# Kernel optimization log

Measured on AMD Instinct MI355X. Metric: run time of the kernel, lower is better.

## Reference

```python
import jax, jax.numpy as jnp
import numpy as np

V = 30000      # vocab_size
D = 300        # t_embed
H = 4          # GATv2 heads
C = 300        # per-head out channels (hidden_dim = t_embed)
HID = 768      # hidden_size
B = 2
T = 800
NEG = 0.2      # GATv2 negative_slope default


def gatv2_layer(x, src, dst, Wl, bl, Wr, br, att, bias):
    """PyG GATv2Conv, eval mode, add_self_loops=True, concat=True.
    x: [N, Fin]; src/dst: [E] (src->dst message flow).
    Wl/Wr: [Fin, H*C]; bl/br: [H*C]; att: [H, C]; bias: [H*C].
    """
    N = x.shape[0]
    xl = (x @ Wl + bl).reshape(N, H, C)   # source transform
    xr = (x @ Wr + br).reshape(N, H, C)   # target transform
    loops = jnp.arange(N)
    s = jnp.concatenate([src, loops])
    d = jnp.concatenate([dst, loops])
    e = jax.nn.leaky_relu(xl[s] + xr[d], NEG)          # [E', H, C]
    logits = jnp.einsum('ehc,hc->eh', e, att)           # [E', H]
    # scatter-softmax over incoming edges per target node
    mx = jax.ops.segment_max(logits, d, num_segments=N)  # [N, H]
    ex = jnp.exp(logits - mx[d])
    den = jax.ops.segment_sum(ex, d, num_segments=N)
    alpha = ex / den[d]                                   # [E', H]
    out = jax.ops.segment_sum(alpha[:, :, None] * xl[s], d, num_segments=N)
    return out.reshape(N, H * C) + bias


def setup_inputs() -> dict:
    key = jax.random.key(0)
    ks = jax.random.split(key, 20)
    sc = 0.05
    inp = {
        'kg_enc_input': jax.random.randint(ks[0], (B, T, 3), 0, V),
        'embeddings': jax.random.normal(ks[1], (V, D), jnp.float32),
        # conv1: GATv2Conv(D, C, heads=H)
        'Wl1': jax.random.normal(ks[2], (D, H * C), jnp.float32) * sc,
        'bl1': jnp.zeros((H * C,), jnp.float32),
        'Wr1': jax.random.normal(ks[3], (D, H * C), jnp.float32) * sc,
        'br1': jnp.zeros((H * C,), jnp.float32),
        'att1': jax.random.normal(ks[4], (H, C), jnp.float32) * sc,
        'bias1': jnp.zeros((H * C,), jnp.float32),
        # conv2: GATv2Conv(4*C, C, heads=H)
        'Wl2': jax.random.normal(ks[5], (H * C, H * C), jnp.float32) * sc,
        'bl2': jnp.zeros((H * C,), jnp.float32),
        'Wr2': jax.random.normal(ks[6], (H * C, H * C), jnp.float32) * sc,
        'br2': jnp.zeros((H * C,), jnp.float32),
        'att2': jax.random.normal(ks[7], (H, C), jnp.float32) * sc,
        'bias2': jnp.zeros((H * C,), jnp.float32),
        # post_mp: Linear(4*C, C) -> Dropout -> Linear(C, D)
        'Wp1': jax.random.normal(ks[8], (H * C, C), jnp.float32) * sc,
        'bp1': jnp.zeros((C,), jnp.float32),
        'Wp2': jax.random.normal(ks[9], (C, D), jnp.float32) * sc,
        'bp2': jnp.zeros((D,), jnp.float32),
        # lii: Linear(3*D, HID, bias=False)
        'Wlii': jax.random.normal(ks[10], (3 * D, HID), jnp.float32) * sc,
    }
    return inp


def reference(kg_enc_input, embeddings, Wl1, bl1, Wr1, br1, att1, bias1,
              Wl2, bl2, Wr2, br2, att2, bias2, Wp1, bp1, Wp2, bp2, Wlii):
    # original GAT.forward detaches x -> no grad to embedding table
    x0 = jax.lax.stop_gradient(embeddings)

    def per_sample(kg):  # kg: [T, 3]
        head, rel, tail = kg[:, 0], kg[:, 1], kg[:, 2]
        # edge_list = cat([[head;rel], [rel;tail]], dim=1)
        src = jnp.concatenate([head, rel])
        dst = jnp.concatenate([rel, tail])
        h = gatv2_layer(x0, src, dst, Wl1, bl1, Wr1, br1, att1, bias1)
        h = jax.nn.relu(h)                 # dropout: eval mode, identity
        h = gatv2_layer(h, src, dst, Wl2, bl2, Wr2, br2, att2, bias2)
        h = jax.nn.relu(h)
        w = (h @ Wp1 + bp1) @ Wp2 + bp2    # post_mp, [V, D]
        # per-triple gather + concat of (h, r, t) node embeddings
        return jnp.concatenate([w[head], w[rel], w[tail]], axis=-1)  # [T, 3D]

    final = jax.vmap(per_sample)(kg_enc_input)   # [B, T, 3D]
    return final @ Wlii                           # [B, T, HID]
```

## Files before the change

kernel.cpp:

```cpp
#include <hip/hip_runtime.h>
#include <hip/hip_bf16.h>

#define V 30000
#define D 300
#define H 4
#define C 300
#define HC 1200
#define B 2
#define T 800
#define E 1600
#define MAXM 2400
#define NEG 0.2f
#define SCAN_CH ((MAXM + 255) / 256)

#define MR 2432
#define KD 320
#define KHC 1216
#define NLR 2432
#define WB_LD 320
#define KF2 960
#define FRW 896

typedef __attribute__((ext_vector_type(8))) unsigned short u16x8;
typedef __attribute__((ext_vector_type(8))) short s16x8;
typedef __attribute__((ext_vector_type(4))) float f32x4;

__device__ inline unsigned short f2b(float v) {
    unsigned u = __float_as_uint(v);
    unsigned r = (u + 0x7FFFu + ((u >> 16) & 1u)) >> 16;
    return (unsigned short)r;
}
__device__ inline float b2f(unsigned short u) {
    return __uint_as_float(((unsigned)u) << 16);
}

#define GLOAD_LDS16(g, l) __builtin_amdgcn_global_load_lds( \
    (const __attribute__((address_space(1))) void*)(g), \
    (__attribute__((address_space(3))) void*)(l), 16, 0, 0)


__global__ void k_init(int* map, int* list, int* deg, int* fill, int* mcnt) {
    int i = blockIdx.x * blockDim.x + threadIdx.x;
    if (i < B * V) map[i] = -1;
    if (i < B * MAXM) { list[i] = 0; deg[i] = 0; fill[i] = 0; }
    if (i < B) mcnt[i] = 0;
}

__global__ void k_mark(const int* __restrict__ kg, int* map) {
    int i = blockIdx.x * blockDim.x + threadIdx.x;
    if (i >= B * T * 3) return;
    int b = i / (T * 3);
    map[b * V + kg[i]] = 1;
}

__global__ void k_compact(int* map, int* list, int* mcnt) {
    int b = blockIdx.y;
    int i = blockIdx.x * 256 + threadIdx.x;
    bool pred = (i < V) && (map[b * V + i] == 1);
    unsigned long long m = __ballot(pred);
    int lane = threadIdx.x & 63;
    int wid = threadIdx.x >> 6;
    __shared__ int wcnt[4];
    __shared__ int base;
    if (lane == 0) wcnt[wid] = __popcll(m);
    __syncthreads();
    if (threadIdx.x == 0) {
        int t = 0;
#pragma unroll
        for (int w2 = 0; w2 < 4; ++w2) { int c = wcnt[w2]; wcnt[w2] = t; t += c; }
        base = t ? atomicAdd(&mcnt[b], t) : 0;
    }
    __syncthreads();
    if (pred) {
        int idx = base + wcnt[wid] + __popcll(m & ((1ull << lane) - 1ull));
        map[b * V + i] = idx;
        list[b * MAXM + idx] = i;
    }
}

__global__ void k_edges(const int* __restrict__ kg, const int* __restrict__ map,
                        int* esrc, int* edst, int* deg, int* tric) {
    int i = blockIdx.x * blockDim.x + threadIdx.x;
    if (i >= B * T) return;
    int b = i / T, t = i % T;
    const int* kk = kg + ((long)b * T + t) * 3;
    int hc = map[b * V + kk[0]];
    int rc = map[b * V + kk[1]];
    int tc = map[b * V + kk[2]];
    int eb = b * E;
    esrc[eb + t]     = hc;  edst[eb + t]     = rc;
    esrc[eb + T + t] = rc;  edst[eb + T + t] = tc;
    atomicAdd(&deg[b * MAXM + rc], 1);
    atomicAdd(&deg[b * MAXM + tc], 1);
    int* tr = tric + ((long)b * T + t) * 3;
    tr[0] = hc; tr[1] = rc; tr[2] = tc;
}

__global__ void k_scan(const int* __restrict__ deg, int* __restrict__ off) {
    int b = blockIdx.x;
    deg += b * MAXM; off += b * (MAXM + 1);
    __shared__ int ts[256];
    int t = threadIdx.x;
    int base = t * SCAN_CH;
    int loc[SCAN_CH];
    int sum = 0;
#pragma unroll
    for (int j = 0; j < SCAN_CH; ++j) {
        int v = (base + j < MAXM) ? deg[base + j] : 0;
        sum += v; loc[j] = sum;
    }
    ts[t] = sum; __syncthreads();
    for (int s = 1; s < 256; s <<= 1) {
        int v = (t >= s) ? ts[t - s] : 0;
        __syncthreads();
        ts[t] += v;
        __syncthreads();
    }
    int excl = (t > 0) ? ts[t - 1] : 0;
#pragma unroll
    for (int j = 0; j < SCAN_CH; ++j)
        if (base + j < MAXM) off[base + j + 1] = excl + loc[j];
    if (t == 0) off[0] = 0;
}

__global__ void k_scatter(const int* __restrict__ esrc, const int* __restrict__ edst,
                          const int* __restrict__ off, int* fill, int* csr) {
    int i = blockIdx.x * blockDim.x + threadIdx.x;
    if (i >= B * E) return;
    int b = i / E;
    int d = edst[i];
    int pos = off[b * (MAXM + 1) + d] + atomicAdd(&fill[b * MAXM + d], 1);
    csr[b * E + pos] = esrc[i];
}

__global__ void k_wt_all(const float* __restrict__ Wl1, const float* __restrict__ Wr1,
                         const float* __restrict__ Wl2, const float* __restrict__ Wr2,
                         const float* __restrict__ Wp1, const float* __restrict__ Wp2,
                         const float* __restrict__ Wlii,
                         const float* __restrict__ bl1, const float* __restrict__ br1,
                         const float* __restrict__ bl2, const float* __restrict__ br2,
                         const float* __restrict__ bp1, const float* __restrict__ bp2,
                         unsigned short* Wlr1t, unsigned short* Wlr2t,
                         unsigned short* Wp2t, unsigned short* Wp1b,
                         unsigned short* Wft2,
                         float* blr1, float* blr2, float* bp12) {
    const int KT[6]  = {10, 10, 38, 38, 10, 30};
    const int CUM[10] = {0, 380, 760, 2204, 3648, 3748, 4468, 4508, 4518, 4520};
    int bid = blockIdx.x;
    int task = 0;
    while (bid >= CUM[task + 1]) ++task;
    int local = bid - CUM[task];
    int tx = threadIdx.x, ty = threadIdx.y;
    int tid = ty * 32 + tx;

    if (task == 6) {
        int r0 = local * 32;
#pragma unroll
        for (int p = 0; p < 4; ++p) {
            int row = r0 + ty + p * 8;
#pragma unroll
            for (int j = 0; j < 10; ++j) {
                int c = tx + j * 32;
                unsigned short v = 0;
                if (row < 1200 && c < 300) v = f2b(Wp1[(long)row * 300 + c]);
                Wp1b[(long)row * 320 + c] = v;
            }
        }
        return;
    }
    if (task == 7) {
        int c = local * 256 + tid;
        if (c < NLR) {
            float v1 = 0.f, v2 = 0.f;
            if (c < 1200) { v1 = bl1[c]; v2 = bl2[c]; }
            else if (c >= 1216 && c < 2416) { v1 = br1[c - 1216]; v2 = br2[c - 1216]; }
            blr1[c] = v1; blr2[c] = v2;
        }
        return;
    }
    if (task == 8) {
        int n = local * 256 + tid;
        if (n < 300) {
            float s = bp2[n];
            for (int m = 0; m < 300; ++m) s += bp1[m] * Wp2[(long)m * 300 + n];
            bp12[n] = s;
        }
        return;
    }

    __shared__ float t[32][33];
    if (task == 5) {
        int kt = local % 30, nt = local / 30;
        int k0 = kt * 32, n0 = nt * 32;
#pragma unroll
        for (int p = 0; p < 4; ++p) {
            int gk = k0 + ty + p * 8, n = n0 + tx;
            int pp = (gk >= 640) ? 2 : (gk >= 320 ? 1 : 0);
            int kc = gk - pp * 320;
            t[ty + p * 8][tx] = (kc < 300) ? Wlii[(long)(300 * pp + kc) * 768 + n] : 0.f;
        }
        __syncthreads();
#pragma unroll
        for (int p = 0; p < 4; ++p) {
            int n = n0 + ty + p * 8, gk = k0 + tx;
            Wft2[(long)n * 960 + gk] = f2b(t[tx][ty + p * 8]);
        }
        return;
    }

    int kt = local % KT[task], nt = local / KT[task];
    const float* W; unsigned short* Wt; int K, N, Kp;
    switch (task) {
        case 0: W = Wl1;  Wt = Wlr1t;                     K = 300;  N = 1200; Kp = KD;  break;
        case 1: W = Wr1;  Wt = Wlr1t + (long)1216 * KD;   K = 300;  N = 1200; Kp = KD;  break;
        case 2: W = Wl2;  Wt = Wlr2t;                     K = 1200; N = 1200; Kp = KHC; break;
        case 3: W = Wr2;  Wt = Wlr2t + (long)1216 * KHC;  K = 1200; N = 1200; Kp = KHC; break;
        default: W = Wp2; Wt = Wp2t;                      K = 300;  N = 300;  Kp = KD;  break;
    }
    int k0 = kt * 32, n0 = nt * 32;
#pragma unroll
    for (int p = 0; p < 4; ++p) {
        int k = k0 + ty + p * 8, n = n0 + tx;
        t[ty + p * 8][tx] = (k < K && n < N) ? W[(long)k * N + n] : 0.f;
    }
    __syncthreads();
#pragma unroll
    for (int p = 0; p < 4; ++p) {
        int n = n0 + ty + p * 8, k = k0 + tx;
        Wt[(long)n * Kp + k] = f2b(t[tx][ty + p * 8]);
    }
}

__global__ void k_embgather(const float* __restrict__ emb, const int* __restrict__ list,
                            unsigned short* __restrict__ Eb) {
    int b = blockIdx.y, i = blockIdx.x;
    int src = list[b * MAXM + i];
    const float* e = emb + (long)src * D;
    unsigned short* o = Eb + ((long)b * MR + i) * KD;
    int c = threadIdx.x;
    if (c < 75) {
        float4 v = *(const float4*)(e + c * 4);
        ushort4 u;
        u.x = f2b(v.x); u.y = f2b(v.y); u.z = f2b(v.z); u.w = f2b(v.w);
        *(ushort4*)(o + c * 4) = u;
    } else if (c < 80) {
        *(ushort4*)(o + c * 4) = make_ushort4(0, 0, 0, 0);
    }
}

__device__ inline void tile_decode(int& m0, int& n0) {
    int nbx = gridDim.x, nby = gridDim.y;
    int nwg = nbx * nby;
    int wg = blockIdx.y * nbx + blockIdx.x;
    int q = nwg >> 3, r8 = nwg & 7;
    int xcd = wg & 7, idx = wg >> 3;
    int L = (xcd < r8 ? xcd * (q + 1) : r8 * (q + 1) + (xcd - r8) * q) + idx;
    const int G = 4;
    int band = L / (G * nbx);
    int first = band * G;
    int sz = min(G, nby - first);
    int rem = L - band * G * nbx;
    int by = first + rem % sz;
    int bx = rem / sz;
    m0 = by * 128; n0 = bx * 128;
}

__global__ __launch_bounds__(256) void k_mgemm(
    const unsigned short* __restrict__ A, long sA, int lda,
    const unsigned short* __restrict__ Wt, int ldw,
    const float* __restrict__ bias,
    int M, int N, int K,
    float* __restrict__ outF, long sF, int ldf,
    unsigned short* __restrict__ outB, long sB, int ldb_) {
    int b = blockIdx.z;
    A += (long)b * sA;
    __shared__ unsigned short As[128][32];
    __shared__ unsigned short Bs[128][32];
    int tid = threadIdx.x;
    int m0, n0; tile_decode(m0, n0);

    int w = tid >> 6, lane = tid & 63;
    int wr = (w >> 1) * 64, wc = (w & 1) * 64;
    int fr = lane & 15, fq = lane >> 4;
    int r0 = tid >> 2, sg = tid & 3;
    int swz = (sg ^ ((r0 >> 1) & 3)) * 8;
    const unsigned short* Ap  = A  + (long)(m0 + r0) * lda + swz;
    const unsigned short* Ap2 = A  + (long)(m0 + r0 + 64) * lda + swz;
    const unsigned short* Bp  = Wt + (long)(n0 + r0) * ldw + swz;
    const unsigned short* Bp2 = Wt + (long)(n0 + r0 + 64) * ldw + swz;
    unsigned short* lA  = &As[r0][sg * 8];
    unsigned short* lA2 = &As[r0 + 64][sg * 8];
    unsigned short* lB  = &Bs[r0][sg * 8];
    unsigned short* lB2 = &Bs[r0 + 64][sg * 8];

    f32x4 acc[4][4] = {};
    for (int k0 = 0; k0 < K; k0 += 32) {
        GLOAD_LDS16(Ap + k0, lA);
        GLOAD_LDS16(Ap2 + k0, lA2);
        GLOAD_LDS16(Bp + k0, lB);
        GLOAD_LDS16(Bp2 + k0, lB2);
        __syncthreads();
        s16x8 af[4], bfr[4];
#pragma unroll
        for (int m = 0; m < 4; ++m) {
            int rr = wr + m * 16 + fr;
            af[m] = *(const s16x8*)&As[rr][(fq ^ ((rr >> 1) & 3)) * 8];
        }
#pragma unroll
        for (int n = 0; n < 4; ++n) {
            int rr = wc + n * 16 + fr;
            bfr[n] = *(const s16x8*)&Bs[rr][(fq ^ ((rr >> 1) & 3)) * 8];
        }
#pragma unroll
        for (int m = 0; m < 4; ++m)
#pragma unroll
            for (int n = 0; n < 4; ++n)
                acc[m][n] = __builtin_amdgcn_mfma_f32_16x16x32_bf16(af[m], bfr[n], acc[m][n], 0, 0, 0);
        __syncthreads();
    }
    float* oF = outF ? outF + (long)b * sF : nullptr;
    unsigned short* oB = outB ? outB + (long)b * sB : nullptr;
#pragma unroll
    for (int m = 0; m < 4; ++m) {
        int rb = m0 + wr + m * 16 + fq * 4;
#pragma unroll
        for (int n = 0; n < 4; ++n) {
            int col = n0 + wc + n * 16 + fr;
#pragma unroll
            for (int j = 0; j < 4; ++j) {
                int row = rb + j;
                if (row >= M) continue;
                if (col < N) {
                    float v = acc[m][n][j] + (bias ? bias[col] : 0.f);
                    if (oF) oF[(long)row * ldf + col] = v;
                    if (oB) oB[(long)row * ldb_ + col] = f2b(v);
                } else if (oB && col < ldb_) {
                    oB[(long)row * ldb_ + col] = 0;
                }
            }
        }
    }
}

__global__ __launch_bounds__(256) void k_fgemm(
    const unsigned short* __restrict__ wb, long sW,
    const int* __restrict__ tric,
    const unsigned short* __restrict__ Wft2,
    float* __restrict__ out) {
    int b = blockIdx.z;
    const unsigned short* wB = wb + (long)b * sW;
    const int* tr = tric + (long)b * T * 3;
    float* oF = out + (long)b * T * 768;
    __shared__ unsigned short As[128][32];
    __shared__ unsigned short Bs[128][32];
    int tid = threadIdx.x;
    int m0, n0; tile_decode(m0, n0);

    int w = tid >> 6, lane = tid & 63;
    int wr = (w >> 1) * 64, wc = (w & 1) * 64;
    int fr = lane & 15, fq = lane >> 4;
    int r0 = tid >> 2, sg = tid & 3;
    int swz = (sg ^ ((r0 >> 1) & 3)) * 8;

    int gm  = m0 + r0;
    int gm2 = gm + 64;
    int t1 = min(gm, T - 1) * 3, t2 = min(gm2, T - 1) * 3;
    int tr0a = tr[t1], tr1a = tr[t1 + 1], tr2a = tr[t1 + 2];
    int tr0b = tr[t2], tr1b = tr[t2 + 1], tr2b = tr[t2 + 2];

    const unsigned short* Bp  = Wft2 + (long)(n0 + r0) * KF2 + swz;
    const unsigned short* Bp2 = Wft2 + (long)(n0 + r0 + 64) * KF2 + swz;
    unsigned short* lA  = &As[r0][sg * 8];
    unsigned short* lA2 = &As[r0 + 64][sg * 8];
    unsigned short* lB  = &Bs[r0][sg * 8];
    unsigned short* lB2 = &Bs[r0 + 64][sg * 8];

    f32x4 acc[4][4] = {};
    for (int k0 = 0; k0 < KF2; k0 += 32) {
        int kk = k0 + swz;
        int p_ = (kk >= 640) ? 2 : (kk >= 320 ? 1 : 0);
        int kc = kk - p_ * 320;
        int tA  = (p_ == 0) ? tr0a : (p_ == 1 ? tr1a : tr2a);
        int tA2 = (p_ == 0) ? tr0b : (p_ == 1 ? tr1b : tr2b);
        GLOAD_LDS16(wB + (long)tA * WB_LD + kc, lA);
        GLOAD_LDS16(wB + (long)tA2 * WB_LD + kc, lA2);
        GLOAD_LDS16(Bp + k0, lB);
        GLOAD_LDS16(Bp2 + k0, lB2);
        __syncthreads();
        s16x8 af[4], bfr[4];
#pragma unroll
        for (int m = 0; m < 4; ++m) {
            int rr = wr + m * 16 + fr;
            af[m] = *(const s16x8*)&As[rr][(fq ^ ((rr >> 1) & 3)) * 8];
        }
#pragma unroll
        for (int n = 0; n < 4; ++n) {
            int rr = wc + n * 16 + fr;
            bfr[n] = *(const s16x8*)&Bs[rr][(fq ^ ((rr >> 1) & 3)) * 8];
        }
#pragma unroll
        for (int m = 0; m < 4; ++m)
#pragma unroll
            for (int n = 0; n < 4; ++n)
                acc[m][n] = __builtin_amdgcn_mfma_f32_16x16x32_bf16(af[m], bfr[n], acc[m][n], 0, 0, 0);
        __syncthreads();
    }
#pragma unroll
    for (int m = 0; m < 4; ++m) {
        int rb = m0 + wr + m * 16 + fq * 4;
#pragma unroll
        for (int n = 0; n < 4; ++n) {
            int col = n0 + wc + n * 16 + fr;
#pragma unroll
            for (int j = 0; j < 4; ++j) {
                int row = rb + j;
                if (row < T) oF[(long)row * 768 + col] = acc[m][n][j];
            }
        }
    }
}

__global__ __launch_bounds__(256) void k_att(
    const unsigned short* __restrict__ XLR,
    const int* __restrict__ deg, const int* __restrict__ off, const int* __restrict__ csr,
    const float* __restrict__ att, const float* __restrict__ bias,
    unsigned short* __restrict__ OUT) {
    const long sX = (long)MR * NLR;
    const long sO = (long)MR * KHC;
    int b = blockIdx.y;
    int i = blockIdx.x;
    const unsigned short* xl = XLR + (long)b * sX;
    const unsigned short* xr = xl + 1216;
    unsigned short* out = OUT + (long)b * sO;
    int lane = threadIdx.x & 63;
    int h = threadIdx.x >> 6;
    int c0 = lane * 4;
    int c1 = 256 + c0;
    bool tail = lane < 11;

    float xrf[8], attf[8];
    {
        const unsigned short* xp = xr + (long)i * NLR + h * C;
        ushort4 u0 = *(const ushort4*)(xp + c0);
        ushort4 u1 = tail ? *(const ushort4*)(xp + c1) : make_ushort4(0, 0, 0, 0);
        xrf[0] = b2f(u0.x); xrf[1] = b2f(u0.y); xrf[2] = b2f(u0.z); xrf[3] = b2f(u0.w);
        xrf[4] = b2f(u1.x); xrf[5] = b2f(u1.y); xrf[6] = b2f(u1.z); xrf[7] = b2f(u1.w);
        float4 a0 = *(const float4*)(att + h * C + c0);
        attf[0] = a0.x; attf[1] = a0.y; attf[2] = a0.z; attf[3] = a0.w;
        if (tail) {
            float4 a1 = *(const float4*)(att + h * C + c1);
            attf[4] = a1.x; attf[5] = a1.y; attf[6] = a1.z; attf[7] = a1.w;
        } else { attf[4] = attf[5] = attf[6] = attf[7] = 0.f; }
    }
    int dg = deg[b * MAXM + i];
    int o0 = off[b * (MAXM + 1) + i];
    const int* cs = csr + b * E;

    float mx = -3e38f, den = 0.f;
    float acc[8] = {0.f, 0.f, 0.f, 0.f, 0.f, 0.f, 0.f, 0.f};
    auto step = [&](int s) {
        const unsigned short* xp = xl + (long)s * NLR + h * C;
        ushort4 v0 = *(const ushort4*)(xp + c0);
        ushort4 v1 = tail ? *(const ushort4*)(xp + c1) : make_ushort4(0, 0, 0, 0);
        float xv[8];
        xv[0] = b2f(v0.x); xv[1] = b2f(v0.y); xv[2] = b2f(v0.z); xv[3] = b2f(v0.w);
        xv[4] = b2f(v1.x); xv[5] = b2f(v1.y); xv[6] = b2f(v1.z); xv[7] = b2f(v1.w);
        float part = 0.f;
#pragma unroll
        for (int j = 0; j < 8; ++j) {
            float v = xv[j] + xrf[j];
            v = v > 0.f ? v : NEG * v;
            part += attf[j] * v;
        }
#pragma unroll
        for (int m = 1; m < 64; m <<= 1) part += __shfl_xor(part, m);
        float mn = fmaxf(mx, part);
        float sc = __expf(mx - mn);
        float p = __expf(part - mn);
        den = den * sc + p;
#pragma unroll
        for (int j = 0; j < 8; ++j) acc[j] = acc[j] * sc + p * xv[j];
        mx = mn;
    };
    step(i);
    for (int e = 0; e < dg; ++e) step(cs[o0 + e]);

    float inv = 1.f / den;
    unsigned short* op = out + (long)i * KHC + h * C;
    {
        float4 b0 = *(const float4*)(bias + h * C + c0);
        ushort4 s0;
        float v;
        v = acc[0] * inv + b0.x; s0.x = f2b(v > 0.f ? v : 0.f);
        v = acc[1] * inv + b0.y; s0.y = f2b(v > 0.f ? v : 0.f);
        v = acc[2] * inv + b0.z; s0.z = f2b(v > 0.f ? v : 0.f);
        v = acc[3] * inv + b0.w; s0.w = f2b(v > 0.f ? v : 0.f);
        *(ushort4*)(op + c0) = s0;
        if (tail) {
            float4 b1 = *(const float4*)(bias + h * C + c1);
            ushort4 s1;
            v = acc[4] * inv + b1.x; s1.x = f2b(v > 0.f ? v : 0.f);
            v = acc[5] * inv + b1.y; s1.y = f2b(v > 0.f ? v : 0.f);
            v = acc[6] * inv + b1.z; s1.z = f2b(v > 0.f ? v : 0.f);
            v = acc[7] * inv + b1.w; s1.w = f2b(v > 0.f ? v : 0.f);
            *(ushort4*)(op + c1) = s1;
        }
    }
    if (h == 0 && lane < KHC - HC)
        out[(long)i * KHC + HC + lane] = 0;
}

extern "C" void kernel_launch(void* const* d_in, const int* in_sizes, int n_in,
                              void* d_out, int out_size, void* d_ws, size_t ws_size,
                              hipStream_t stream) {
    const int*   kg    = (const int*)d_in[0];
    const float* emb   = (const float*)d_in[1];
    const float* Wl1   = (const float*)d_in[2];
    const float* bl1   = (const float*)d_in[3];
    const float* Wr1   = (const float*)d_in[4];
    const float* br1   = (const float*)d_in[5];
    const float* att1  = (const float*)d_in[6];
    const float* bias1 = (const float*)d_in[7];
    const float* Wl2   = (const float*)d_in[8];
    const float* bl2   = (const float*)d_in[9];
    const float* Wr2   = (const float*)d_in[10];
    const float* br2   = (const float*)d_in[11];
    const float* att2  = (const float*)d_in[12];
    const float* bias2 = (const float*)d_in[13];
    const float* Wp1   = (const float*)d_in[14];
    const float* bp1   = (const float*)d_in[15];
    const float* Wp2   = (const float*)d_in[16];
    const float* bp2   = (const float*)d_in[17];
    const float* Wlii  = (const float*)d_in[18];
    float* out = (float*)d_out;

    char* ws = (char*)d_ws;
    size_t o = 0;
    auto alloc = [&](size_t bytes) -> void* {
        void* p = ws + o;
        o = (o + bytes + 255) & ~(size_t)255;
        return p;
    };
    int* map  = (int*)alloc(sizeof(int) * B * V);
    int* list = (int*)alloc(sizeof(int) * B * MAXM);
    int* mcnt = (int*)alloc(sizeof(int) * B);
    int* deg  = (int*)alloc(sizeof(int) * B * MAXM);
    int* off  = (int*)alloc(sizeof(int) * B * (MAXM + 1));
    int* fill = (int*)alloc(sizeof(int) * B * MAXM);
    int* esrc = (int*)alloc(sizeof(int) * B * E);
    int* edst = (int*)alloc(sizeof(int) * B * E);
    int* csr  = (int*)alloc(sizeof(int) * B * E);
    int* tric = (int*)alloc(sizeof(int) * B * T * 3);

    long sXlr = (long)MR * NLR;
    long sHb  = (long)MR * KHC;
    long sEb  = (long)MR * KD;
    unsigned short* Xlr = (unsigned short*)alloc(2LL * B * sXlr);
    unsigned short* Hb  = (unsigned short*)alloc(2LL * B * sHb);
    unsigned short* Eb  = (unsigned short*)alloc(2LL * B * sEb);

    unsigned short* Wlr1t = (unsigned short*)alloc(2LL * 2432 * KD);
    unsigned short* Wlr2t = (unsigned short*)alloc(2LL * 2432 * KHC);
    unsigned short* Wp2t  = (unsigned short*)alloc(2LL * 384 * KD);
    unsigned short* Wp1b  = (unsigned short*)alloc(2LL * 1280 * 320);
    unsigned short* Wp12t = (unsigned short*)alloc(2LL * 384 * KHC);
    unsigned short* Wft2  = (unsigned short*)alloc(2LL * 768 * KF2);
    float* blr1 = (float*)alloc(sizeof(float) * NLR);
    float* blr2 = (float*)alloc(sizeof(float) * NLR);
    float* bp12 = (float*)alloc(sizeof(float) * 384);
    (void)ws_size; (void)in_sizes; (void)n_in; (void)out_size;

    unsigned short* wb = Eb;

    k_init<<<(B * V + 255) / 256, 256, 0, stream>>>(map, list, deg, fill, mcnt);
    k_mark<<<(B * T * 3 + 255) / 256, 256, 0, stream>>>(kg, map);
    k_compact<<<dim3((V + 255) / 256, B), 256, 0, stream>>>(map, list, mcnt);
    k_edges<<<(B * T + 255) / 256, 256, 0, stream>>>(kg, map, esrc, edst, deg, tric);
    k_scan<<<B, 256, 0, stream>>>(deg, off);
    k_scatter<<<(B * E + 255) / 256, 256, 0, stream>>>(esrc, edst, off, fill, csr);

    k_wt_all<<<4520, dim3(32, 8), 0, stream>>>(Wl1, Wr1, Wl2, Wr2, Wp1, Wp2, Wlii,
                                               bl1, br1, bl2, br2, bp1, bp2,
                                               Wlr1t, Wlr2t, Wp2t, Wp1b, Wft2,
                                               blr1, blr2, bp12);

    k_embgather<<<dim3(MAXM, B), 128, 0, stream>>>(emb, list, Eb);

    k_mgemm<<<dim3(10, 3, 1), 256, 0, stream>>>(Wp2t, 0, KD, Wp1b, 320, nullptr,
                                                300, 1216, KD,
                                                nullptr, 0, 0, Wp12t, 0, KHC);

    long sWb = (long)MR * WB_LD;

    dim3 gL(19, 19, B);
    k_mgemm<<<gL, 256, 0, stream>>>(Eb, sEb, KD, Wlr1t, KD, blr1, MAXM, NLR, KD,
                                    nullptr, 0, 0, Xlr, sXlr, NLR);
    k_att<<<dim3(MAXM, B), 256, 0, stream>>>(Xlr, deg, off, csr, att1, bias1, Hb);
    k_mgemm<<<gL, 256, 0, stream>>>(Hb, sHb, KHC, Wlr2t, KHC, blr2, MAXM, NLR, KHC,
                                    nullptr, 0, 0, Xlr, sXlr, NLR);
    k_att<<<dim3(MAXM, B), 256, 0, stream>>>(Xlr, deg, off, csr, att2, bias2, Hb);
    k_mgemm<<<dim3(3, 19, B), 256, 0, stream>>>(Hb, sHb, KHC, Wp12t, KHC, bp12,
                                                MAXM, 300, KHC,
                                                nullptr, 0, 0, wb, sWb, WB_LD);
    k_fgemm<<<dim3(6, 7, B), 256, 0, stream>>>(wb, sWb, tric, Wft2, out);
}
```

Baseline: 346.4 us.

## Fuse graph CSR build into one kernel and double-buffer GEMM LDS tiles

Replaces the separate edge, scan and scatter kernels with one per-batch kernel that builds degrees, offsets and the CSR in shared memory, which drops two launches and the global atomics and buffers. The attention kernel now derives degree from consecutive offsets. Both GEMM kernels switch to double-buffered LDS so the next K-slice's global-to-LDS loads are issued before computing on the current one, aiming to overlap memory latency with MFMA work. This doubles LDS use per block, which may lower occupancy, and the fused graph kernel runs on only B blocks.

```diff
diff --git a/kernel.cpp b/kernel.cpp
--- a/kernel.cpp
+++ b/kernel.cpp
@@ -19,7 +19,6 @@
 #define NLR 2432
 #define WB_LD 320
 #define KF2 960
-#define FRW 896
 
 typedef __attribute__((ext_vector_type(8))) unsigned short u16x8;
 typedef __attribute__((ext_vector_type(8))) short s16x8;
@@ -39,10 +38,10 @@
     (__attribute__((address_space(3))) void*)(l), 16, 0, 0)
 
 
-__global__ void k_init(int* map, int* list, int* deg, int* fill, int* mcnt) {
+__global__ void k_init(int* map, int* list, int* mcnt) {
     int i = blockIdx.x * blockDim.x + threadIdx.x;
     if (i < B * V) map[i] = -1;
-    if (i < B * MAXM) { list[i] = 0; deg[i] = 0; fill[i] = 0; }
+    if (i < B * MAXM) list[i] = 0;
     if (i < B) mcnt[i] = 0;
 }
 
@@ -78,59 +77,62 @@
     }
 }
 
-__global__ void k_edges(const int* __restrict__ kg, const int* __restrict__ map,
-                        int* esrc, int* edst, int* deg, int* tric) {
-    int i = blockIdx.x * blockDim.x + threadIdx.x;
-    if (i >= B * T) return;
-    int b = i / T, t = i % T;
-    const int* kk = kg + ((long)b * T + t) * 3;
-    int hc = map[b * V + kk[0]];
-    int rc = map[b * V + kk[1]];
-    int tc = map[b * V + kk[2]];
-    int eb = b * E;
-    esrc[eb + t]     = hc;  edst[eb + t]     = rc;
-    esrc[eb + T + t] = rc;  edst[eb + T + t] = tc;
-    atomicAdd(&deg[b * MAXM + rc], 1);
-    atomicAdd(&deg[b * MAXM + tc], 1);
-    int* tr = tric + ((long)b * T + t) * 3;
-    tr[0] = hc; tr[1] = rc; tr[2] = tc;
-}
-
-__global__ void k_scan(const int* __restrict__ deg, int* __restrict__ off) {
+__global__ __launch_bounds__(256) void k_graph(const int* __restrict__ kg,
+                                               const int* __restrict__ map,
+                                               int* __restrict__ off_g,
+                                               int* __restrict__ csr,
+                                               int* __restrict__ tric) {
     int b = blockIdx.x;
-    deg += b * MAXM; off += b * (MAXM + 1);
+    int tid = threadIdx.x;
+    __shared__ int sdeg[MAXM];
+    __shared__ int soff[MAXM + 1];
+    __shared__ int ses[E];
+    __shared__ int sed[E];
     __shared__ int ts[256];
-    int t = threadIdx.x;
-    int base = t * SCAN_CH;
+    for (int j = tid; j < MAXM; j += 256) sdeg[j] = 0;
+    __syncthreads();
+    for (int t = tid; t < T; t += 256) {
+        const int* kk = kg + ((long)b * T + t) * 3;
+        int hc = map[b * V + kk[0]];
+        int rc = map[b * V + kk[1]];
+        int tc = map[b * V + kk[2]];
+        ses[t] = hc;     sed[t] = rc;
+        ses[T + t] = rc; sed[T + t] = tc;
+        atomicAdd(&sdeg[rc], 1);
+        atomicAdd(&sdeg[tc], 1);
+        int* tr = tric + ((long)b * T + t) * 3;
+        tr[0] = hc; tr[1] = rc; tr[2] = tc;
+    }
+    __syncthreads();
+    int base = tid * SCAN_CH;
     int loc[SCAN_CH];
     int sum = 0;
 #pragma unroll
     for (int j = 0; j < SCAN_CH; ++j) {
-        int v = (base + j < MAXM) ? deg[base + j] : 0;
+        int v = (base + j < MAXM) ? sdeg[base + j] : 0;
         sum += v; loc[j] = sum;
     }
-    ts[t] = sum; __syncthreads();
+    ts[tid] = sum; __syncthreads();
     for (int s = 1; s < 256; s <<= 1) {
-        int v = (t >= s) ? ts[t - s] : 0;
+        int v = (tid >= s) ? ts[tid - s] : 0;
         __syncthreads();
-        ts[t] += v;
+        ts[tid] += v;
         __syncthreads();
     }
-    int excl = (t > 0) ? ts[t - 1] : 0;
+    int excl = (tid > 0) ? ts[tid - 1] : 0;
 #pragma unroll
     for (int j = 0; j < SCAN_CH; ++j)
-        if (base + j < MAXM) off[base + j + 1] = excl + loc[j];
-    if (t == 0) off[0] = 0;
-}
-
-__global__ void k_scatter(const int* __restrict__ esrc, const int* __restrict__ edst,
-                          const int* __restrict__ off, int* fill, int* csr) {
-    int i = blockIdx.x * blockDim.x + threadIdx.x;
-    if (i >= B * E) return;
-    int b = i / E;
-    int d = edst[i];
-    int pos = off[b * (MAXM + 1) + d] + atomicAdd(&fill[b * MAXM + d], 1);
-    csr[b * E + pos] = esrc[i];
+        if (base + j < MAXM) soff[base + j + 1] = excl + loc[j];
+    if (tid == 0) soff[0] = 0;
+    __syncthreads();
+    for (int j = tid; j < MAXM; j += 256) sdeg[j] = 0;
+    __syncthreads();
+    for (int e = tid; e < E; e += 256) {
+        int d = sed[e];
+        int pos = soff[d] + atomicAdd(&sdeg[d], 1);
+        csr[b * E + pos] = ses[e];
+    }
+    for (int j = tid; j <= MAXM; j += 256) off_g[b * (MAXM + 1) + j] = soff[j];
 }
 
 __global__ void k_wt_all(const float* __restrict__ Wl1, const float* __restrict__ Wr1,
@@ -274,8 +276,8 @@
     unsigned short* __restrict__ outB, long sB, int ldb_) {
     int b = blockIdx.z;
     A += (long)b * sA;
-    __shared__ unsigned short As[128][32];
-    __shared__ unsigned short Bs[128][32];
+    __shared__ unsigned short As[2][128][32];
+    __shared__ unsigned short Bs[2][128][32];
     int tid = threadIdx.x;
     int m0, n0; tile_decode(m0, n0);
 
@@ -288,28 +290,32 @@
     const unsigned short* Ap2 = A  + (long)(m0 + r0 + 64) * lda + swz;
     const unsigned short* Bp  = Wt + (long)(n0 + r0) * ldw + swz;
     const unsigned short* Bp2 = Wt + (long)(n0 + r0 + 64) * ldw + swz;
-    unsigned short* lA  = &As[r0][sg * 8];
-    unsigned short* lA2 = &As[r0 + 64][sg * 8];
-    unsigned short* lB  = &Bs[r0][sg * 8];
-    unsigned short* lB2 = &Bs[r0 + 64][sg * 8];
 
     f32x4 acc[4][4] = {};
+    GLOAD_LDS16(Ap,  &As[0][r0][sg * 8]);
+    GLOAD_LDS16(Ap2, &As[0][r0 + 64][sg * 8]);
+    GLOAD_LDS16(Bp,  &Bs[0][r0][sg * 8]);
+    GLOAD_LDS16(Bp2, &Bs[0][r0 + 64][sg * 8]);
+    __syncthreads();
+    int cur = 0;
     for (int k0 = 0; k0 < K; k0 += 32) {
-        GLOAD_LDS16(Ap + k0, lA);
-        GLOAD_LDS16(Ap2 + k0, lA2);
-        GLOAD_LDS16(Bp + k0, lB);
-        GLOAD_LDS16(Bp2 + k0, lB2);
-        __syncthreads();
+        int nxt = cur ^ 1;
+        if (k0 + 32 < K) {
+            GLOAD_LDS16(Ap + k0 + 32,  &As[nxt][r0][sg * 8]);
+            GLOAD_LDS16(Ap2 + k0 + 32, &As[nxt][r0 + 64][sg * 8]);
+            GLOAD_LDS16(Bp + k0 + 32,  &Bs[nxt][r0][sg * 8]);
+            GLOAD_LDS16(Bp2 + k0 + 32, &Bs[nxt][r0 + 64][sg * 8]);
+        }
         s16x8 af[4], bfr[4];
 #pragma unroll
         for (int m = 0; m < 4; ++m) {
             int rr = wr + m * 16 + fr;
-            af[m] = *(const s16x8*)&As[rr][(fq ^ ((rr >> 1) & 3)) * 8];
+            af[m] = *(const s16x8*)&As[cur][rr][(fq ^ ((rr >> 1) & 3)) * 8];
         }
 #pragma unroll
         for (int n = 0; n < 4; ++n) {
             int rr = wc + n * 16 + fr;
-            bfr[n] = *(const s16x8*)&Bs[rr][(fq ^ ((rr >> 1) & 3)) * 8];
+            bfr[n] = *(const s16x8*)&Bs[cur][rr][(fq ^ ((rr >> 1) & 3)) * 8];
         }
 #pragma unroll
         for (int m = 0; m < 4; ++m)
@@ -317,6 +323,7 @@
             for (int n = 0; n < 4; ++n)
                 acc[m][n] = __builtin_amdgcn_mfma_f32_16x16x32_bf16(af[m], bfr[n], acc[m][n], 0, 0, 0);
         __syncthreads();
+        cur = nxt;
     }
     float* oF = outF ? outF + (long)b * sF : nullptr;
     unsigned short* oB = outB ? outB + (long)b * sB : nullptr;
@@ -351,8 +358,8 @@
     const unsigned short* wB = wb + (long)b * sW;
     const int* tr = tric + (long)b * T * 3;
     float* oF = out + (long)b * T * 768;
-    __shared__ unsigned short As[128][32];
-    __shared__ unsigned short Bs[128][32];
+    __shared__ unsigned short As[2][128][32];
+    __shared__ unsigned short Bs[2][128][32];
     int tid = threadIdx.x;
     int m0, n0; tile_decode(m0, n0);
 
@@ -365,38 +372,39 @@
     int gm  = m0 + r0;
     int gm2 = gm + 64;
     int t1 = min(gm, T - 1) * 3, t2 = min(gm2, T - 1) * 3;
-    int tr0a = tr[t1], tr1a = tr[t1 + 1], tr2a = tr[t1 + 2];
-    int tr0b = tr[t2], tr1b = tr[t2 + 1], tr2b = tr[t2 + 2];
+    int tr_a[3] = {tr[t1], tr[t1 + 1], tr[t1 + 2]};
+    int tr_b[3] = {tr[t2], tr[t2 + 1], tr[t2 + 2]};
 
     const unsigned short* Bp  = Wft2 + (long)(n0 + r0) * KF2 + swz;
     const unsigned short* Bp2 = Wft2 + (long)(n0 + r0 + 64) * KF2 + swz;
-    unsigned short* lA  = &As[r0][sg * 8];
-    unsigned short* lA2 = &As[r0 + 64][sg * 8];
-    unsigned short* lB  = &Bs[r0][sg * 8];
-    unsigned short* lB2 = &Bs[r0 + 64][sg * 8];
-
-    f32x4 acc[4][4] = {};
-    for (int k0 = 0; k0 < KF2; k0 += 32) {
+
+    auto stage = [&](int buf, int k0) {
         int kk = k0 + swz;
         int p_ = (kk >= 640) ? 2 : (kk >= 320 ? 1 : 0);
         int kc = kk - p_ * 320;
-        int tA  = (p_ == 0) ? tr0a : (p_ == 1 ? tr1a : tr2a);
-        int tA2 = (p_ == 0) ? tr0b : (p_ == 1 ? tr1b : tr2b);
-        GLOAD_LDS16(wB + (long)tA * WB_LD + kc, lA);
-        GLOAD_LDS16(wB + (long)tA2 * WB_LD + kc, lA2);
-        GLOAD_LDS16(Bp + k0, lB);
-        GLOAD_LDS16(Bp2 + k0, lB2);
-        __syncthreads();
+        GLOAD_LDS16(wB + (long)tr_a[p_] * WB_LD + kc, &As[buf][r0][sg * 8]);
+        GLOAD_LDS16(wB + (long)tr_b[p_] * WB_LD + kc, &As[buf][r0 + 64][sg * 8]);
+        GLOAD_LDS16(Bp + k0,  &Bs[buf][r0][sg * 8]);
+        GLOAD_LDS16(Bp2 + k0, &Bs[buf][r0 + 64][sg * 8]);
+    };
+
+    f32x4 acc[4][4] = {};
+    stage(0, 0);
+    __syncthreads();
+    int cur = 0;
+    for (int k0 = 0; k0 < KF2; k0 += 32) {
+        int nxt = cur ^ 1;
+        if (k0 + 32 < KF2) stage(nxt, k0 + 32);
         s16x8 af[4], bfr[4];
 #pragma unroll
         for (int m = 0; m < 4; ++m) {
             int rr = wr + m * 16 + fr;
-            af[m] = *(const s16x8*)&As[rr][(fq ^ ((rr >> 1) & 3)) * 8];
+            af[m] = *(const s16x8*)&As[cur][rr][(fq ^ ((rr >> 1) & 3)) * 8];
         }
 #pragma unroll
         for (int n = 0; n < 4; ++n) {
             int rr = wc + n * 16 + fr;
-            bfr[n] = *(const s16x8*)&Bs[rr][(fq ^ ((rr >> 1) & 3)) * 8];
+            bfr[n] = *(const s16x8*)&Bs[cur][rr][(fq ^ ((rr >> 1) & 3)) * 8];
         }
 #pragma unroll
         for (int m = 0; m < 4; ++m)
@@ -404,6 +412,7 @@
             for (int n = 0; n < 4; ++n)
                 acc[m][n] = __builtin_amdgcn_mfma_f32_16x16x32_bf16(af[m], bfr[n], acc[m][n], 0, 0, 0);
         __syncthreads();
+        cur = nxt;
     }
 #pragma unroll
     for (int m = 0; m < 4; ++m) {
@@ -422,7 +431,7 @@
 
 __global__ __launch_bounds__(256) void k_att(
     const unsigned short* __restrict__ XLR,
-    const int* __restrict__ deg, const int* __restrict__ off, const int* __restrict__ csr,
+    const int* __restrict__ off, const int* __restrict__ csr,
     const float* __restrict__ att, const float* __restrict__ bias,
     unsigned short* __restrict__ OUT) {
     const long sX = (long)MR * NLR;
@@ -452,8 +461,8 @@
             attf[4] = a1.x; attf[5] = a1.y; attf[6] = a1.z; attf[7] = a1.w;
         } else { attf[4] = attf[5] = attf[6] = attf[7] = 0.f; }
     }
-    int dg = deg[b * MAXM + i];
     int o0 = off[b * (MAXM + 1) + i];
+    int dg = off[b * (MAXM + 1) + i + 1] - o0;
     const int* cs = csr + b * E;
 
     float mx = -3e38f, den = 0.f;
@@ -544,11 +553,7 @@
     int* map  = (int*)alloc(sizeof(int) * B * V);
     int* list = (int*)alloc(sizeof(int) * B * MAXM);
     int* mcnt = (int*)alloc(sizeof(int) * B);
-    int* deg  = (int*)alloc(sizeof(int) * B * MAXM);
     int* off  = (int*)alloc(sizeof(int) * B * (MAXM + 1));
-    int* fill = (int*)alloc(sizeof(int) * B * MAXM);
-    int* esrc = (int*)alloc(sizeof(int) * B * E);
-    int* edst = (int*)alloc(sizeof(int) * B * E);
     int* csr  = (int*)alloc(sizeof(int) * B * E);
     int* tric = (int*)alloc(sizeof(int) * B * T * 3);
 
@@ -572,12 +577,10 @@
 
     unsigned short* wb = Eb;
 
-    k_init<<<(B * V + 255) / 256, 256, 0, stream>>>(map, list, deg, fill, mcnt);
+    k_init<<<(B * V + 255) / 256, 256, 0, stream>>>(map, list, mcnt);
     k_mark<<<(B * T * 3 + 255) / 256, 256, 0, stream>>>(kg, map);
     k_compact<<<dim3((V + 255) / 256, B), 256, 0, stream>>>(map, list, mcnt);
-    k_edges<<<(B * T + 255) / 256, 256, 0, stream>>>(kg, map, esrc, edst, deg, tric);
-    k_scan<<<B, 256, 0, stream>>>(deg, off);
-    k_scatter<<<(B * E + 255) / 256, 256, 0, stream>>>(esrc, edst, off, fill, csr);
+    k_graph<<<B, 256, 0, stream>>>(kg, map, off, csr, tric);
 
     k_wt_all<<<4520, dim3(32, 8), 0, stream>>>(Wl1, Wr1, Wl2, Wr2, Wp1, Wp2, Wlii,
                                                bl1, br1, bl2, br2, bp1, bp2,
@@ -595,10 +598,10 @@
     dim3 gL(19, 19, B);
     k_mgemm<<<gL, 256, 0, stream>>>(Eb, sEb, KD, Wlr1t, KD, blr1, MAXM, NLR, KD,
                                     nullptr, 0, 0, Xlr, sXlr, NLR);
-    k_att<<<dim3(MAXM, B), 256, 0, stream>>>(Xlr, deg, off, csr, att1, bias1, Hb);
+    k_att<<<dim3(MAXM, B), 256, 0, stream>>>(Xlr, off, csr, att1, bias1, Hb);
     k_mgemm<<<gL, 256, 0, stream>>>(Hb, sHb, KHC, Wlr2t, KHC, blr2, MAXM, NLR, KHC,
                                     nullptr, 0, 0, Xlr, sXlr, NLR);
-    k_att<<<dim3(MAXM, B), 256, 0, stream>>>(Xlr, deg, off, csr, att2, bias2, Hb);
+    k_att<<<dim3(MAXM, B), 256, 0, stream>>>(Xlr, off, csr, att2, bias2, Hb);
     k_mgemm<<<dim3(3, 19, B), 256, 0, stream>>>(Hb, sHb, KHC, Wp12t, KHC, bp12,
                                                 MAXM, 300, KHC,
                                                 nullptr, 0, 0, wb, sWb, WB_LD);
```

After: 328.5 us. 5.2% less time.
